# Kernel tuning notes

Hardware: AMD Instinct MI355X
Metric: run time of the kernel (lower is better)

## Reference

```python
import jax, jax.numpy as jnp
import numpy as np

N_HEAD = 16


def setup_inputs() -> dict:
    key = jax.random.key(0)
    ks = jax.random.split(key, 4)
    B, T, C = 4, 2048, 1024
    x = jax.random.normal(ks[0], (B, T, C), dtype=jnp.float32)
    w_qkv = jax.random.normal(ks[1], (C, 3 * C), dtype=jnp.float32) * (1.0 / np.sqrt(C))
    b_qkv = jnp.zeros((3 * C,), dtype=jnp.float32)
    w_out = jax.random.normal(ks[2], (C, C), dtype=jnp.float32) * (1.0 / np.sqrt(C))
    b_out = jnp.zeros((C,), dtype=jnp.float32)
    return {"x": x, "w_qkv": w_qkv, "b_qkv": b_qkv, "w_out": w_out, "b_out": b_out}


def reference(x, w_qkv, b_qkv, w_out, b_out):
    B, T, C = x.shape
    H = N_HEAD
    D = C // H  # head_dim
    qkv = x @ w_qkv + b_qkv                      # [B,T,3C]
    q, k, v = jnp.split(qkv, 3, axis=-1)
    # [B,T,C] -> [B,H,T,D]
    q = q.reshape(B, T, H, D).transpose(0, 2, 1, 3)
    k = k.reshape(B, T, H, D).transpose(0, 2, 1, 3)
    v = v.reshape(B, T, H, D).transpose(0, 2, 1, 3)
    scores = jnp.einsum('bhqd,bhkd->bhqk', q, k) / jnp.sqrt(jnp.float32(D))
    causal = jnp.tril(jnp.ones((T, T), dtype=bool))
    scores = jnp.where(causal, scores, jnp.float32(-jnp.inf))
    attn = jax.nn.softmax(scores, axis=-1)       # dropout omitted (eval, p=0)
    out = jnp.einsum('bhqk,bhkd->bhqd', attn, v)
    out = out.transpose(0, 2, 1, 3).reshape(B, T, C)
    out = out @ w_out + b_out
    return out
```

## Files before the change

### kernel.cpp

```cpp
#include <hip/hip_runtime.h>
#include <hip/hip_bf16.h>

typedef unsigned short u16;
typedef unsigned int u32;
typedef __attribute__((ext_vector_type(8))) __bf16 bhalf8;
typedef __attribute__((ext_vector_type(8))) u16 us8;
typedef __attribute__((ext_vector_type(4))) u16 us4;
typedef __attribute__((ext_vector_type(4))) float f32x4;

#if __has_builtin(__builtin_amdgcn_mfma_f32_16x16x16_bf16)
typedef __attribute__((ext_vector_type(4))) __bf16 bhalf4;
#define MFMA16(a, b, c) __builtin_amdgcn_mfma_f32_16x16x16_bf16(a, b, c, 0, 0, 0)
#else
typedef __attribute__((ext_vector_type(4))) short bhalf4;
#define MFMA16(a, b, c) __builtin_amdgcn_mfma_f32_16x16x16bf16_1k(a, b, c, 0, 0, 0)
#endif

__device__ __forceinline__ u16 bf16rne(float f) {
  u32 u = __float_as_uint(f);
  u += 0x7FFFu + ((u >> 16) & 1u);
  return (u16)(u >> 16);
}

__device__ __forceinline__ u32 pkbf(float a, float b) {
  union { __hip_bfloat162 h; u32 w; } u;
  u.h = __float22bfloat162_rn(make_float2(a, b));
  return u.w;
}

__global__ __launch_bounds__(256) void cast4_kernel(const float* __restrict__ in,
                                                    u16* __restrict__ out, int n) {
  int i = (blockIdx.x * 256 + threadIdx.x) * 4;
  if (i >= n) return;
  float4 f = *(const float4*)(in + i);
  u32 lo = pkbf(f.x, f.y);
  u32 hi = pkbf(f.z, f.w);
  *(uint2*)(out + i) = make_uint2(lo, hi);
}

__global__ __launch_bounds__(256) void transpose_cast_kernel(const float* __restrict__ in,
                                                             u16* __restrict__ out,
                                                             int R, int Cn) {
  __shared__ float tile[32][33];
  int c0 = blockIdx.x * 32, r0 = blockIdx.y * 32;
  int tx = threadIdx.x, ty = threadIdx.y;
#pragma unroll
  for (int j = 0; j < 4; ++j)
    tile[ty + j * 8][tx] = in[(size_t)(r0 + ty + j * 8) * Cn + c0 + tx];
  __syncthreads();
#pragma unroll
  for (int j = 0; j < 4; ++j)
    out[(size_t)(c0 + ty + j * 8) * R + r0 + tx] = bf16rne(tile[tx][ty + j * 8]);
}

template <int MODE>
__global__ __launch_bounds__(256, 2) void gemm_bt_kernel(
    const u16* __restrict__ A, const u16* __restrict__ Bt, const float* __restrict__ bias,
    float* __restrict__ outf, u16* __restrict__ qb, u16* __restrict__ kb, u16* __restrict__ vb,
    int Mdim, int Ndim, int Kdim) {
  __shared__ __align__(16) u16 lA[128 * 64];
  __shared__ __align__(16) u16 lB[128 * 64];
  const int tid = threadIdx.x;
  const int lane = tid & 63;
  const int col = lane & 15, quad = lane >> 4;
  const int wid = tid >> 6;
  const int m0 = blockIdx.y * 128, n0 = blockIdx.x * 128;
  const int wm = (wid >> 1) * 64, wn = (wid & 1) * 64;

  f32x4 acc[4][4];
#pragma unroll
  for (int i = 0; i < 4; ++i)
#pragma unroll
    for (int j = 0; j < 4; ++j) acc[i][j] = f32x4{0.f, 0.f, 0.f, 0.f};

  for (int k0 = 0; k0 < Kdim; k0 += 64) {
    const u16* Ag = A + (size_t)m0 * Kdim + k0;
    const u16* Bg = Bt + (size_t)n0 * Kdim + k0;
#pragma unroll
    for (int r = 0; r < 4; ++r) {
      int c = r * 256 + tid;
      int row = c >> 3;
      int bblk = (c & 7) ^ (row & 7);
      size_t ldsoff = (size_t)(r * 256 + (tid & 0xC0)) * 8;
      __builtin_amdgcn_global_load_lds(
          (const __attribute__((address_space(1))) void*)(Ag + (size_t)row * Kdim + bblk * 8),
          (__attribute__((address_space(3))) void*)(lA + ldsoff), 16, 0, 0);
      __builtin_amdgcn_global_load_lds(
          (const __attribute__((address_space(1))) void*)(Bg + (size_t)row * Kdim + bblk * 8),
          (__attribute__((address_space(3))) void*)(lB + ldsoff), 16, 0, 0);
    }
    __syncthreads();
#pragma unroll
    for (int ks = 0; ks < 2; ++ks) {
      bhalf8 af[4], bfr[4];
#pragma unroll
      for (int i = 0; i < 4; ++i) {
        int ra = wm + i * 16 + col;
        int rb = wn + i * 16 + col;
        af[i]  = *(const bhalf8*)&lA[ra * 64 + (((ks * 4 + quad) ^ (ra & 7)) * 8)];
        bfr[i] = *(const bhalf8*)&lB[rb * 64 + (((ks * 4 + quad) ^ (rb & 7)) * 8)];
      }
#pragma unroll
      for (int mt = 0; mt < 4; ++mt)
#pragma unroll
        for (int nt = 0; nt < 4; ++nt)
          acc[mt][nt] = __builtin_amdgcn_mfma_f32_16x16x32_bf16(af[mt], bfr[nt], acc[mt][nt], 0, 0, 0);
    }
    __syncthreads();
  }

  if (MODE == 0) {
#pragma unroll
    for (int nt = 0; nt < 4; ++nt) {
      int n = n0 + wn + nt * 16 + col;
      float bv = bias[n];
      int which = n >> 10, cc = n & 1023, hh = cc >> 6, dd = cc & 63;
      if (which == 2) {
#pragma unroll
        for (int mt = 0; mt < 4; ++mt) {
          int t0 = m0 + wm + mt * 16 + quad * 4;
          int bb = t0 >> 11, tt = t0 & 2047;
          us4 w;
#pragma unroll
          for (int reg = 0; reg < 4; ++reg) w[reg] = bf16rne(acc[mt][nt][reg] + bv);
          *(us4*)(vb + ((size_t)(bb * 16 + hh) * 64 + dd) * 2048 + tt) = w;
        }
      } else {
        u16* dst = which ? kb : qb;
#pragma unroll
        for (int mt = 0; mt < 4; ++mt)
#pragma unroll
          for (int reg = 0; reg < 4; ++reg) {
            int m = m0 + wm + mt * 16 + quad * 4 + reg;
            int bb = m >> 11, tt = m & 2047;
            dst[((size_t)(bb * 16 + hh) * 2048 + tt) * 64 + dd] = bf16rne(acc[mt][nt][reg] + bv);
          }
      }
    }
  } else {
#pragma unroll
    for (int mt = 0; mt < 4; ++mt)
#pragma unroll
      for (int nt = 0; nt < 4; ++nt) {
        int n = n0 + wn + nt * 16 + col;
        float bv = bias[n];
#pragma unroll
        for (int reg = 0; reg < 4; ++reg) {
          int m = m0 + wm + mt * 16 + quad * 4 + reg;
          outf[(size_t)m * Ndim + n] = acc[mt][nt][reg] + bv;
        }
      }
  }
}

__global__ __launch_bounds__(256, 2) void attn_kernel(const u16* __restrict__ Q,
                                                      const u16* __restrict__ K,
                                                      const u16* __restrict__ VT,
                                                      u16* __restrict__ aout) {
  __shared__ __align__(16) u16 lK[2][128 * 64];
  __shared__ __align__(16) u16 lV[2][64 * 128];
  const int tid = threadIdx.x;
  const int lane = tid & 63, wid = tid >> 6;
  const int col = lane & 15, quad = lane >> 4;
  const int bh = blockIdx.y;
  const int b = bh >> 4, h = bh & 15;
  const u16* Qb = Q + (size_t)bh * 2048 * 64;
  const u16* Kb = K + (size_t)bh * 2048 * 64;
  const u16* Vb = VT + (size_t)bh * 64 * 2048;
  const float CS = 0.18033688011112042f;
  const int qbase = wid * 32;
  const int wuni = (tid & 0xC0);

  for (int phase = 0; phase < 2; ++phase) {
    const int qt = (phase == 0) ? (15 - (int)blockIdx.x) : (int)blockIdx.x;

    auto stage = [&](int kt, int bufi) {
      const u16* Kg = Kb + (size_t)kt * 128 * 64;
      const u16* Vg = Vb + (size_t)kt * 128;
#pragma unroll
      for (int r = 0; r < 4; ++r) {
        int c = r * 256 + tid;
        size_t ldsoff = (size_t)(r * 256 + wuni) * 8;
        int krow = c >> 3, kblk = (c & 7) ^ (krow & 7);
        __builtin_amdgcn_global_load_lds(
            (const __attribute__((address_space(1))) void*)(Kg + (size_t)krow * 64 + kblk * 8),
            (__attribute__((address_space(3))) void*)(&lK[bufi][0] + ldsoff), 16, 0, 0);
        int vrow = c >> 4, vblk = (c & 15) ^ (vrow & 15);
        __builtin_amdgcn_global_load_lds(
            (const __attribute__((address_space(1))) void*)(Vg + (size_t)vrow * 2048 + vblk * 8),
            (__attribute__((address_space(3))) void*)(&lV[bufi][0] + ldsoff), 16, 0, 0);
      }
    };

    bhalf8 qf[2][2];
#pragma unroll
    for (int ntq = 0; ntq < 2; ++ntq)
#pragma unroll
      for (int ks = 0; ks < 2; ++ks)
        qf[ntq][ks] = *(const bhalf8*)(Qb + (size_t)(qt * 128 + qbase + ntq * 16 + col) * 64 +
                                       ks * 32 + quad * 8);

    f32x4 oacc[4][2];
    float lr[2] = {0.f, 0.f};
#pragma unroll
    for (int dt = 0; dt < 4; ++dt)
#pragma unroll
      for (int ntq = 0; ntq < 2; ++ntq) oacc[dt][ntq] = f32x4{0.f, 0.f, 0.f, 0.f};

    stage(0, 0);

    for (int kt = 0; kt <= qt; ++kt) {
      const int cur = kt & 1;
      __syncthreads();
      if (kt < qt) stage(kt + 1, cur ^ 1);
      const bool diag = (kt == qt);
      const int ntkhi = diag ? (2 * wid + 2) : 8;

      f32x4 sacc[8][2];
#pragma unroll
      for (int ntk = 0; ntk < 8; ++ntk)
#pragma unroll
        for (int ntq = 0; ntq < 2; ++ntq) sacc[ntk][ntq] = f32x4{0.f, 0.f, 0.f, 0.f};
#pragma unroll
      for (int ks = 0; ks < 2; ++ks) {
        bhalf8 kf[8];
#pragma unroll
        for (int ntk = 0; ntk < 8; ++ntk)
          if (ntk < ntkhi) {
            int ra = ntk * 16 + col;
            kf[ntk] = *(const bhalf8*)&lK[cur][ra * 64 + (((ks * 4 + quad) ^ (ra & 7)) * 8)];
          }
#pragma unroll
        for (int ntk = 0; ntk < 8; ++ntk)
          if (ntk < ntkhi) {
#pragma unroll
            for (int ntq = 0; ntq < 2; ++ntq)
              sacc[ntk][ntq] = __builtin_amdgcn_mfma_f32_16x16x32_bf16(kf[ntk], qf[ntq][ks],
                                                                       sacc[ntk][ntq], 0, 0, 0);
          }
      }

      if (diag) {
#pragma unroll
        for (int ntk = 0; ntk < 8; ++ntk)
          if (ntk >= 2 * wid && ntk < 2 * wid + 2) {
#pragma unroll
            for (int ntq = 0; ntq < 2; ++ntq) {
              int qloc = qbase + ntq * 16 + col;
#pragma unroll
              for (int reg = 0; reg < 4; ++reg) {
                int kloc = ntk * 16 + quad * 4 + reg;
                if (kloc > qloc) sacc[ntk][ntq][reg] = -1e30f;
              }
            }
          }
      }

#pragma unroll
      for (int ntk = 0; ntk < 8; ++ntk)
        if (ntk < ntkhi) {
          bhalf4 vf[4];
#pragma unroll
          for (int dt = 0; dt < 4; ++dt) {
            int vrow = dt * 16 + col;
            vf[dt] = *(const bhalf4*)&lV[cur][vrow * 128 +
                                             (((ntk * 2 + (quad >> 1)) ^ col) * 8) + (quad & 1) * 4];
          }
#pragma unroll
          for (int ntq = 0; ntq < 2; ++ntq) {
            float p0 = exp2f(sacc[ntk][ntq][0] * CS);
            float p1 = exp2f(sacc[ntk][ntq][1] * CS);
            float p2 = exp2f(sacc[ntk][ntq][2] * CS);
            float p3 = exp2f(sacc[ntk][ntq][3] * CS);
            lr[ntq] += (p0 + p1) + (p2 + p3);
            union { u32 w[2]; bhalf4 v; } pfu;
            pfu.w[0] = pkbf(p0, p1);
            pfu.w[1] = pkbf(p2, p3);
#pragma unroll
            for (int dt = 0; dt < 4; ++dt)
              oacc[dt][ntq] = MFMA16(vf[dt], pfu.v, oacc[dt][ntq]);
          }
        }
    }

#pragma unroll
    for (int ntq = 0; ntq < 2; ++ntq) {
      float r = lr[ntq];
      r += __shfl_xor(r, 16);
      r += __shfl_xor(r, 32);
      float inv = 1.f / r;
      int q = qt * 128 + qbase + ntq * 16 + col;
      size_t base = ((size_t)(b * 2048 + q)) * 1024 + h * 64;
#pragma unroll
      for (int dt = 0; dt < 4; ++dt) {
        us4 w;
#pragma unroll
        for (int reg = 0; reg < 4; ++reg) w[reg] = bf16rne(oacc[dt][ntq][reg] * inv);
        *(us4*)(aout + base + dt * 16 + quad * 4) = w;
      }
    }
    __syncthreads();
  }
}

extern "C" void kernel_launch(void* const* d_in, const int* in_sizes, int n_in,
                              void* d_out, int out_size, void* d_ws, size_t ws_size,
                              hipStream_t stream) {
  const float* x     = (const float*)d_in[0];
  const float* w_qkv = (const float*)d_in[1];
  const float* b_qkv = (const float*)d_in[2];
  const float* w_out = (const float*)d_in[3];
  const float* b_out = (const float*)d_in[4];
  float* out = (float*)d_out;
  char* ws = (char*)d_ws;
  u16* xb    = (u16*)(ws);
  u16* wqkvT = (u16*)(ws + 16777216);
  u16* woutT = (u16*)(ws + 23068672);
  u16* qb    = (u16*)(ws + 25165824);
  u16* kb    = (u16*)(ws + 41943040);
  u16* vT    = (u16*)(ws + 58720256);
  u16* ab    = (u16*)(ws + 75497472);

  cast4_kernel<<<8192, 256, 0, stream>>>(x, xb, 8388608);
  dim3 tb(32, 8);
  transpose_cast_kernel<<<dim3(96, 32), tb, 0, stream>>>(w_qkv, wqkvT, 1024, 3072);
  transpose_cast_kernel<<<dim3(32, 32), tb, 0, stream>>>(w_out, woutT, 1024, 1024);
  gemm_bt_kernel<0><<<dim3(24, 64), 256, 0, stream>>>(xb, wqkvT, b_qkv, nullptr, qb, kb, vT,
                                                      8192, 3072, 1024);
  attn_kernel<<<dim3(8, 64), 256, 0, stream>>>(qb, kb, vT, ab);
  gemm_bt_kernel<1><<<dim3(8, 64), 256, 0, stream>>>(ab, woutT, b_out, out, nullptr, nullptr,
                                                     nullptr, 8192, 1024, 1024);
}
```

Measured before the change: 257.6 us.

## Fold softmax scale into Q projection, use raw exp2, remap blocks for L2 locality

The softmax scale (log2e/sqrt(D)) is now applied to Q in the QKV GEMM epilogue, so the attention inner loop drops a multiply per score and calls the hardware exp2 builtin directly instead of exp2f. Both GEMM and attention kernels remap the linear block id into groups of 8 so blocks running at the same time share A/B tiles or heads in L2 (MI355X has 8 XCDs). This relies on the grid shapes (24 or 8 columns, 8 attention blocks per head) being hardcoded. Rounding scaled Q to bf16 changes numerics slightly.

```diff
diff --git a/kernel.cpp b/kernel.cpp
--- a/kernel.cpp
+++ b/kernel.cpp
@@ -14,6 +14,12 @@
 #else
 typedef __attribute__((ext_vector_type(4))) short bhalf4;
 #define MFMA16(a, b, c) __builtin_amdgcn_mfma_f32_16x16x16bf16_1k(a, b, c, 0, 0, 0)
+#endif
+
+#if __has_builtin(__builtin_amdgcn_exp2f)
+#define EXP2(x) __builtin_amdgcn_exp2f(x)
+#else
+#define EXP2(x) exp2f(x)
 #endif
 
 __device__ __forceinline__ u16 bf16rne(float f) {
@@ -64,14 +70,20 @@
   const int lane = tid & 63;
   const int col = lane & 15, quad = lane >> 4;
   const int wid = tid >> 6;
-  const int m0 = blockIdx.y * 128, n0 = blockIdx.x * 128;
+  const int gx = (MODE == 0) ? 24 : 8;
+  int id = blockIdx.y * gx + blockIdx.x;
+  int g = id & 7, j = id >> 3;
+  int vy = g * 8 + j / gx;
+  int vx = j % gx;
+  const int m0 = vy * 128, n0 = vx * 128;
   const int wm = (wid >> 1) * 64, wn = (wid & 1) * 64;
+  const float QSC = 0.18033688011112042f;
 
   f32x4 acc[4][4];
 #pragma unroll
   for (int i = 0; i < 4; ++i)
 #pragma unroll
-    for (int j = 0; j < 4; ++j) acc[i][j] = f32x4{0.f, 0.f, 0.f, 0.f};
+    for (int j2 = 0; j2 < 4; ++j2) acc[i][j2] = f32x4{0.f, 0.f, 0.f, 0.f};
 
   for (int k0 = 0; k0 < Kdim; k0 += 64) {
     const u16* Ag = A + (size_t)m0 * Kdim + k0;
@@ -127,13 +139,14 @@
         }
       } else {
         u16* dst = which ? kb : qb;
+        float sc = which ? 1.0f : QSC;
 #pragma unroll
         for (int mt = 0; mt < 4; ++mt)
 #pragma unroll
           for (int reg = 0; reg < 4; ++reg) {
             int m = m0 + wm + mt * 16 + quad * 4 + reg;
             int bb = m >> 11, tt = m & 2047;
-            dst[((size_t)(bb * 16 + hh) * 2048 + tt) * 64 + dd] = bf16rne(acc[mt][nt][reg] + bv);
+            dst[((size_t)(bb * 16 + hh) * 2048 + tt) * 64 + dd] = bf16rne((acc[mt][nt][reg] + bv) * sc);
           }
       }
     }
@@ -162,17 +175,19 @@
   const int tid = threadIdx.x;
   const int lane = tid & 63, wid = tid >> 6;
   const int col = lane & 15, quad = lane >> 4;
-  const int bh = blockIdx.y;
+  int id = blockIdx.y * 8 + blockIdx.x;
+  int g = id & 7, j = id >> 3;
+  const int bh = g * 8 + (j >> 3);
+  const int bx = j & 7;
   const int b = bh >> 4, h = bh & 15;
   const u16* Qb = Q + (size_t)bh * 2048 * 64;
   const u16* Kb = K + (size_t)bh * 2048 * 64;
   const u16* Vb = VT + (size_t)bh * 64 * 2048;
-  const float CS = 0.18033688011112042f;
   const int qbase = wid * 32;
   const int wuni = (tid & 0xC0);
 
   for (int phase = 0; phase < 2; ++phase) {
-    const int qt = (phase == 0) ? (15 - (int)blockIdx.x) : (int)blockIdx.x;
+    const int qt = (phase == 0) ? (15 - bx) : bx;
 
     auto stage = [&](int kt, int bufi) {
       const u16* Kg = Kb + (size_t)kt * 128 * 64;
@@ -268,10 +283,10 @@
           }
 #pragma unroll
           for (int ntq = 0; ntq < 2; ++ntq) {
-            float p0 = exp2f(sacc[ntk][ntq][0] * CS);
-            float p1 = exp2f(sacc[ntk][ntq][1] * CS);
-            float p2 = exp2f(sacc[ntk][ntq][2] * CS);
-            float p3 = exp2f(sacc[ntk][ntq][3] * CS);
+            float p0 = EXP2(sacc[ntk][ntq][0]);
+            float p1 = EXP2(sacc[ntk][ntq][1]);
+            float p2 = EXP2(sacc[ntk][ntq][2]);
+            float p3 = EXP2(sacc[ntk][ntq][3]);
             lr[ntq] += (p0 + p1) + (p2 + p3);
             union { u32 w[2]; bhalf4 v; } pfu;
             pfu.w[0] = pkbf(p0, p1);
```

Result: faster. 245.8 us (-4.6%).
